# Kernel tuning notes

Hardware: AMD Instinct MI355X
Metric: run time of the kernel (lower is better)

Reference implementation:

```python
import jax, jax.numpy as jnp
import numpy as np

H, W, C_IN, C_OUT, N = 512, 512, 256, 256, 65536


def setup_inputs() -> dict:
    key = jax.random.key(0)
    k1, k2, k3, k4 = jax.random.split(key, 4)
    feature = jax.random.normal(k1, (1, C_IN, H, W), dtype=jnp.float32)
    weight = jax.random.normal(k2, (C_OUT, C_IN, 3, 3), dtype=jnp.float32) * 0.05
    # base sparse locations in the unpadded map; build 3x3 neighborhood indices
    # into the PADDED ([H+2, W+2]) map, exactly like F.pad + fancy indexing.
    base_h = jax.random.randint(k3, (N,), 0, H, dtype=jnp.int32)
    base_w = jax.random.randint(k4, (N,), 0, W, dtype=jnp.int32)
    dh = jnp.repeat(jnp.arange(3, dtype=jnp.int32), 3)  # [9]: 0,0,0,1,1,1,2,2,2
    dw = jnp.tile(jnp.arange(3, dtype=jnp.int32), 3)    # [9]: 0,1,2,0,1,2,...
    h_idx = base_h[None, :] + dh[:, None]  # [9, N], values in [0, H+1]
    w_idx = base_w[None, :] + dw[:, None]  # [9, N], values in [0, W+1]
    return {"feature": feature, "weight": weight, "h_idx": h_idx, "w_idx": w_idx}


def reference(feature, weight, h_idx, w_idx):
    # feature: [1, C, H, W]; weight: [Cout, C, 3, 3]; h_idx/w_idx: [9, N]
    C = feature.shape[1]
    out_ch = weight.shape[0]
    # F.pad(feature, [1,1,1,1])[0] -> [C, H+2, W+2]
    padded = jnp.pad(feature, ((0, 0), (0, 0), (1, 1), (1, 1)))[0]
    # gather 3x3 neighborhoods at sparse locations -> [C, 9, N]
    gathered = padded[:, h_idx, w_idx]
    # .view(9*C, -1): contiguous reshape gives row index c*9 + k
    g = gathered.reshape(C * 9, -1)  # [C*9, N]
    # kernel_d2s = weight.view(out, -1): row ordering c*9 + (kh*3+kw) matches
    k2d = weight.reshape(out_ch, -1)  # [Cout, C*9]
    return k2d @ g  # [Cout, N]
```

## Files before the change

### kernel.cpp

```cpp
#include <hip/hip_runtime.h>
#include <hip/hip_bf16.h>

#define HH 512
#define WW 512
#define CIN 256
#define COUT 256
#define NPTS 65536
#define KTOT 2304
#define PW 514
#define NPIX (PW * PW)

typedef __bf16 bf16x8 __attribute__((ext_vector_type(8)));
typedef float f32x4 __attribute__((ext_vector_type(4)));
typedef unsigned short us8 __attribute__((ext_vector_type(8)));

static __device__ __forceinline__ unsigned short f2bf(float f) {
  unsigned u = __builtin_bit_cast(unsigned, f);
  unsigned r = u + 0x7fffu + ((u >> 16) & 1u);
  return (unsigned short)(r >> 16);
}

static __device__ __forceinline__ void gload16(const void* g, void* l) {
  __builtin_amdgcn_global_load_lds(
      (const __attribute__((address_space(1))) unsigned int*)g,
      (__attribute__((address_space(3))) unsigned int*)l, 16, 0, 0);
}

__global__ __launch_bounds__(256) void prep_weight(const float* __restrict__ w,
                                                   unsigned short* __restrict__ A) {
  int i = blockIdx.x * 256 + threadIdx.x;
  int j  = i & 7;
  int pc = (i >> 3) & 3;
  int co = (i >> 5) & 255;
  int kk = i >> 13;
  int lc = pc ^ ((co >> 1) & 3);
  int k  = kk * 32 + lc * 8 + j;
  int t  = k >> 8;
  int ci = k & 255;
  A[i] = f2bf(w[co * 2304 + ci * 9 + t]);
}

__global__ __launch_bounds__(256) void border_zero(unsigned short* __restrict__ Ft) {
  int g = blockIdx.x * 256 + threadIdx.x;
  if (g >= 2052 * 32) return;
  int p = g >> 5, c = g & 31;
  int py, px;
  if (p < 514)        { py = 0;        px = p; }
  else if (p < 1028)  { py = 513;      px = p - 514; }
  else if (p < 1540)  { py = p - 1027; px = 0; }
  else                { py = p - 1539; px = 513; }
  *(us8*)&Ft[((size_t)py * PW + px) * 256 + c * 8] = (us8){0, 0, 0, 0, 0, 0, 0, 0};
}

__global__ __launch_bounds__(256) void transpose_feat(const float* __restrict__ f,
                                                      unsigned short* __restrict__ Ft) {
  __shared__ unsigned short lds[64 * 264];
  int pix0 = blockIdx.x * 64;
  int y = pix0 >> 9, x0 = pix0 & 511;
  int tid = threadIdx.x;
  int p = tid & 63;
  int cb = tid >> 6;
  const float* src = f + pix0 + p;
  for (int c8 = 0; c8 < 8; ++c8) {
    us8 v;
#pragma unroll
    for (int j = 0; j < 8; ++j) {
      int ci = cb * 64 + c8 * 8 + j;
      v[j] = f2bf(src[ci * 262144]);
    }
    *(us8*)&lds[p * 264 + cb * 64 + c8 * 8] = v;
  }
  __syncthreads();
  int cic = tid & 31;
  int pr = tid >> 5;
  for (int g = 0; g < 8; ++g) {
    int p2 = pr + g * 8;
    us8 v = *(const us8*)&lds[p2 * 264 + cic * 8];
    *(us8*)&Ft[((size_t)((y + 1) * PW + x0 + 1 + p2)) * 256 + cic * 8] = v;
  }
}

__global__ __launch_bounds__(512) void gemm_gather(
    const unsigned short* __restrict__ A,
    const unsigned short* __restrict__ Ft,
    const int* __restrict__ hidx,
    const int* __restrict__ widx,
    float* __restrict__ out) {
  __shared__ unsigned short Asm[2 * 256 * 32];
  __shared__ unsigned short Bsm[2 * 128 * 32];

  int tid = threadIdx.x;
  int n0 = blockIdx.x * 128;
  int lane = tid & 63, wv = tid >> 6;
  int m0 = (wv & 3) * 64;
  int nw0 = (wv >> 2) * 64;

  int col = tid >> 2;
  int pc  = tid & 3;
  int lc  = pc ^ ((col >> 1) & 3);
  int p0  = hidx[n0 + col] * PW + widx[n0 + col];
  const unsigned short* FtT = Ft + (size_t)p0 * 256 + lc * 8;

  f32x4 acc[4][4];
#pragma unroll
  for (int mi = 0; mi < 4; ++mi)
#pragma unroll
    for (int nj = 0; nj < 4; ++nj)
      acc[mi][nj] = (f32x4){0.f, 0.f, 0.f, 0.f};

  unsigned short* AsmW = &Asm[wv * 512];
  unsigned short* BsmW = &Bsm[wv * 512];

#define STAGE(BUF, KK)                                                        \
  do {                                                                        \
    const unsigned short* ga = A + (size_t)(KK) * 8192 + tid * 8;             \
    gload16(ga, AsmW + (BUF) * 8192);                                         \
    gload16(ga + 4096, AsmW + (BUF) * 8192 + 4096);                           \
    int t_ = (KK) >> 3;                                                       \
    int q_ = t_ / 3;                                                          \
    int dt_ = q_ * PW + (t_ - q_ * 3);                                        \
    int ci0_ = ((KK) & 7) * 32;                                               \
    gload16(FtT + (size_t)dt_ * 256 + ci0_, BsmW + (BUF) * 4096);             \
  } while (0)

  STAGE(0, 0);
  __syncthreads();

  int cur = 0;
  for (int kk = 0; kk < 72; ++kk) {
    if (kk + 1 < 72) STAGE(cur ^ 1, kk + 1);

    bf16x8 af[4], bfr[4];
#pragma unroll
    for (int mi = 0; mi < 4; ++mi) {
      int row = m0 + mi * 16 + (lane & 15);
      int ch = (lane >> 4) ^ ((row >> 1) & 3);
      af[mi] = *(const bf16x8*)&Asm[cur * 8192 + row * 32 + ch * 8];
    }
#pragma unroll
    for (int nj = 0; nj < 4; ++nj) {
      int ccol = nw0 + nj * 16 + (lane & 15);
      int ch = (lane >> 4) ^ ((ccol >> 1) & 3);
      bfr[nj] = *(const bf16x8*)&Bsm[cur * 4096 + ccol * 32 + ch * 8];
    }
#pragma unroll
    for (int mi = 0; mi < 4; ++mi)
#pragma unroll
      for (int nj = 0; nj < 4; ++nj)
        acc[mi][nj] = __builtin_amdgcn_mfma_f32_16x16x32_bf16(af[mi], bfr[nj], acc[mi][nj], 0, 0, 0);

    __syncthreads();
    cur ^= 1;
  }
#undef STAGE

  int ocol = n0 + nw0 + (lane & 15);
  int r0 = (lane >> 4) * 4;
#pragma unroll
  for (int mi = 0; mi < 4; ++mi)
#pragma unroll
    for (int nj = 0; nj < 4; ++nj)
#pragma unroll
      for (int r = 0; r < 4; ++r)
        out[(size_t)(m0 + mi * 16 + r0 + r) * NPTS + ocol + nj * 16] = acc[mi][nj][r];
}

__global__ __launch_bounds__(256) void naive_conv(const float* __restrict__ f,
                                                  const float* __restrict__ w,
                                                  const int* __restrict__ hi,
                                                  const int* __restrict__ wi,
                                                  float* __restrict__ out) {
  int idx = blockIdx.x * 256 + threadIdx.x;
  int n = idx & (NPTS - 1);
  int co = idx >> 16;
  int bh = hi[n] - 1;
  int bw = wi[n] - 1;
  float acc = 0.f;
  for (int ci = 0; ci < CIN; ++ci) {
    const float* fc = f + (size_t)ci * 262144;
    const float* wc = w + (size_t)co * 2304 + ci * 9;
#pragma unroll
    for (int t = 0; t < 9; ++t) {
      int y = bh + t / 3, x = bw + t % 3;
      float v = (y >= 0 && y < 512 && x >= 0 && x < 512) ? fc[y * 512 + x] : 0.f;
      acc += wc[t] * v;
    }
  }
  out[(size_t)co * NPTS + n] = acc;
}

extern "C" void kernel_launch(void* const* d_in, const int* in_sizes, int n_in,
                              void* d_out, int out_size, void* d_ws, size_t ws_size,
                              hipStream_t stream) {
  const float* feature = (const float*)d_in[0];
  const float* weight  = (const float*)d_in[1];
  const int* hidx      = (const int*)d_in[2];
  const int* widx      = (const int*)d_in[3];
  float* out           = (float*)d_out;

  const size_t FT_OFF = 2ull * 1024 * 1024;
  const size_t FT_BYTES = (size_t)NPIX * 256 * 2;
  const size_t NEED = FT_OFF + FT_BYTES;

  if (ws_size >= NEED) {
    unsigned short* Abf = (unsigned short*)d_ws;
    unsigned short* Ft = (unsigned short*)((char*)d_ws + FT_OFF);
    prep_weight<<<(72 * 256 * 32) / 256, 256, 0, stream>>>(weight, Abf);
    border_zero<<<(2052 * 32 + 255) / 256, 256, 0, stream>>>(Ft);
    transpose_feat<<<262144 / 64, 256, 0, stream>>>(feature, Ft);
    gemm_gather<<<NPTS / 128, 512, 0, stream>>>(Abf, Ft, hidx, widx, out);
  } else {
    naive_conv<<<(COUT * NPTS) / 256, 256, 0, stream>>>(feature, weight, hidx, widx, out);
  }
}
```

Measured before the change: 191.3 us.

## Enlarge gather-GEMM tile to 256x256 with K=64 steps and interleaved async staging

```diff
diff --git a/kernel.cpp b/kernel.cpp
--- a/kernel.cpp
+++ b/kernel.cpp
@@ -6,9 +6,9 @@
 #define CIN 256
 #define COUT 256
 #define NPTS 65536
-#define KTOT 2304
 #define PW 514
 #define NPIX (PW * PW)
+#define NKT 36
 
 typedef __bf16 bf16x8 __attribute__((ext_vector_type(8)));
 typedef float f32x4 __attribute__((ext_vector_type(4)));
@@ -29,15 +29,17 @@
 __global__ __launch_bounds__(256) void prep_weight(const float* __restrict__ w,
                                                    unsigned short* __restrict__ A) {
   int i = blockIdx.x * 256 + threadIdx.x;
-  int j  = i & 7;
-  int pc = (i >> 3) & 3;
-  int co = (i >> 5) & 255;
-  int kk = i >> 13;
-  int lc = pc ^ ((co >> 1) & 3);
-  int k  = kk * 32 + lc * 8 + j;
+  int kb = i >> 14;
+  int s  = (i >> 13) & 1;
+  int o  = i & 8191;
+  int r  = o >> 5;
+  int cp = (o >> 3) & 3;
+  int j  = o & 7;
+  int c  = cp ^ ((r >> 1) & 3);
+  int k  = kb * 64 + s * 32 + c * 8 + j;
   int t  = k >> 8;
   int ci = k & 255;
-  A[i] = f2bf(w[co * 2304 + ci * 9 + t]);
+  A[i] = f2bf(w[r * 2304 + ci * 9 + t]);
 }
 
 __global__ __launch_bounds__(256) void border_zero(unsigned short* __restrict__ Ft) {
@@ -80,89 +82,152 @@
   }
 }
 
-__global__ __launch_bounds__(512) void gemm_gather(
+__global__ __launch_bounds__(512, 2) void gemm_gather(
     const unsigned short* __restrict__ A,
     const unsigned short* __restrict__ Ft,
     const int* __restrict__ hidx,
     const int* __restrict__ widx,
     float* __restrict__ out) {
-  __shared__ unsigned short Asm[2 * 256 * 32];
-  __shared__ unsigned short Bsm[2 * 128 * 32];
+  __shared__ unsigned short lds[65536];
+  unsigned short* ldsB = lds + 32768;
 
   int tid = threadIdx.x;
-  int n0 = blockIdx.x * 128;
   int lane = tid & 63, wv = tid >> 6;
-  int m0 = (wv & 3) * 64;
-  int nw0 = (wv >> 2) * 64;
-
-  int col = tid >> 2;
-  int pc  = tid & 3;
-  int lc  = pc ^ ((col >> 1) & 3);
-  int p0  = hidx[n0 + col] * PW + widx[n0 + col];
-  const unsigned short* FtT = Ft + (size_t)p0 * 256 + lc * 8;
-
-  f32x4 acc[4][4];
-#pragma unroll
-  for (int mi = 0; mi < 4; ++mi)
+  int wm = wv & 1, wn = wv >> 1;
+  int n0 = blockIdx.x << 8;
+
+  int c0 = tid >> 2;
+  int cc = (tid & 3) ^ ((tid >> 3) & 3);
+  long pixA = (long)hidx[n0 + c0] * PW + widx[n0 + c0];
+  long pixB = (long)hidx[n0 + 128 + c0] * PW + widx[n0 + 128 + c0];
+  const unsigned short* FtB0 = Ft + pixA * 256 + cc * 8;
+  const unsigned short* FtB1 = Ft + pixB * 256 + cc * 8;
+
+#define STAGE_A(dbuf, kb_, s_)                                                \
+  do {                                                                        \
+    const unsigned short* g_ = A + (kb_) * 16384 + (s_) * 8192 + tid * 8;     \
+    unsigned short* l_ = lds + (dbuf) * 16384 + (s_) * 8192 + tid * 8;        \
+    gload16(g_, l_);                                                          \
+    gload16(g_ + 4096, l_ + 4096);                                            \
+  } while (0)
+
+#define STAGE_B(dbuf, s_, base_)                                              \
+  do {                                                                        \
+    unsigned short* l_ = ldsB + (dbuf) * 16384 + (s_) * 8192 + tid * 8;       \
+    gload16(FtB0 + (base_) + (s_) * 32, l_);                                  \
+    gload16(FtB1 + (base_) + (s_) * 32, l_ + 4096);                           \
+  } while (0)
+
+#define LDA(dst, dbuf, s_, mi_)                                               \
+  do {                                                                        \
+    int r_ = wm * 128 + (mi_) * 16 + (lane & 15);                             \
+    int cp_ = (lane >> 4) ^ ((r_ >> 1) & 3);                                  \
+    dst = *(const bf16x8*)&lds[(dbuf) * 16384 + (s_) * 8192 + r_ * 32 + cp_ * 8]; \
+  } while (0)
+
+#define LDB(dst, dbuf, s_, nj_)                                               \
+  do {                                                                        \
+    int col_ = wn * 64 + (nj_) * 16 + (lane & 15);                            \
+    int cp_ = (lane >> 4) ^ ((col_ >> 1) & 3);                                \
+    dst = *(const bf16x8*)&ldsB[(dbuf) * 16384 + (s_) * 8192 + col_ * 32 + cp_ * 8]; \
+  } while (0)
+
+#define MFMA16(mq_)                                                           \
+  do {                                                                        \
+    __builtin_amdgcn_s_setprio(1);                                            \
+    _Pragma("unroll") for (int mi = 0; mi < 4; ++mi)                          \
+        _Pragma("unroll") for (int nj = 0; nj < 4; ++nj)                      \
+            acc[(mq_) * 4 + mi][nj] = __builtin_amdgcn_mfma_f32_16x16x32_bf16( \
+                af[mi], bfr[nj], acc[(mq_) * 4 + mi][nj], 0, 0, 0);           \
+    __builtin_amdgcn_s_setprio(0);                                            \
+  } while (0)
+
+  f32x4 acc[8][4];
+#pragma unroll
+  for (int mi = 0; mi < 8; ++mi)
 #pragma unroll
     for (int nj = 0; nj < 4; ++nj)
       acc[mi][nj] = (f32x4){0.f, 0.f, 0.f, 0.f};
 
-  unsigned short* AsmW = &Asm[wv * 512];
-  unsigned short* BsmW = &Bsm[wv * 512];
-
-#define STAGE(BUF, KK)                                                        \
-  do {                                                                        \
-    const unsigned short* ga = A + (size_t)(KK) * 8192 + tid * 8;             \
-    gload16(ga, AsmW + (BUF) * 8192);                                         \
-    gload16(ga + 4096, AsmW + (BUF) * 8192 + 4096);                           \
-    int t_ = (KK) >> 3;                                                       \
-    int q_ = t_ / 3;                                                          \
-    int dt_ = q_ * PW + (t_ - q_ * 3);                                        \
-    int ci0_ = ((KK) & 7) * 32;                                               \
-    gload16(FtT + (size_t)dt_ * 256 + ci0_, BsmW + (BUF) * 4096);             \
-  } while (0)
-
-  STAGE(0, 0);
-  __syncthreads();
-
-  int cur = 0;
-  for (int kk = 0; kk < 72; ++kk) {
-    if (kk + 1 < 72) STAGE(cur ^ 1, kk + 1);
+  STAGE_A(0, 0, 0);
+  STAGE_B(0, 0, 0);
+  STAGE_A(0, 0, 1);
+  STAGE_B(0, 1, 0);
+  asm volatile("s_waitcnt vmcnt(4)" ::: "memory");
+  __builtin_amdgcn_s_barrier();
+
+  for (int kb = 0; kb < NKT - 1; ++kb) {
+    int d = kb & 1;
+    int kn = kb + 1;
+    int tp = kn >> 2;
+    int q3 = tp / 3;
+    int dtb = (q3 * PW + (tp - q3 * 3)) * 256 + (kn & 3) * 64;
 
     bf16x8 af[4], bfr[4];
-#pragma unroll
-    for (int mi = 0; mi < 4; ++mi) {
-      int row = m0 + mi * 16 + (lane & 15);
-      int ch = (lane >> 4) ^ ((row >> 1) & 3);
-      af[mi] = *(const bf16x8*)&Asm[cur * 8192 + row * 32 + ch * 8];
-    }
-#pragma unroll
-    for (int nj = 0; nj < 4; ++nj) {
-      int ccol = nw0 + nj * 16 + (lane & 15);
-      int ch = (lane >> 4) ^ ((ccol >> 1) & 3);
-      bfr[nj] = *(const bf16x8*)&Bsm[cur * 4096 + ccol * 32 + ch * 8];
-    }
-#pragma unroll
-    for (int mi = 0; mi < 4; ++mi)
-#pragma unroll
-      for (int nj = 0; nj < 4; ++nj)
-        acc[mi][nj] = __builtin_amdgcn_mfma_f32_16x16x32_bf16(af[mi], bfr[nj], acc[mi][nj], 0, 0, 0);
-
-    __syncthreads();
-    cur ^= 1;
-  }
-#undef STAGE
-
-  int ocol = n0 + nw0 + (lane & 15);
+    LDA(af[0], d, 0, 0); LDA(af[1], d, 0, 1); LDA(af[2], d, 0, 2); LDA(af[3], d, 0, 3);
+    LDB(bfr[0], d, 0, 0); LDB(bfr[1], d, 0, 1); LDB(bfr[2], d, 0, 2); LDB(bfr[3], d, 0, 3);
+    STAGE_A(d ^ 1, kn, 0);
+    __builtin_amdgcn_s_barrier();
+    MFMA16(0);
+    __builtin_amdgcn_s_barrier();
+    LDA(af[0], d, 0, 4); LDA(af[1], d, 0, 5); LDA(af[2], d, 0, 6); LDA(af[3], d, 0, 7);
+    STAGE_B(d ^ 1, 0, dtb);
+    __builtin_amdgcn_s_barrier();
+    MFMA16(1);
+    asm volatile("s_waitcnt vmcnt(4)" ::: "memory");
+    __builtin_amdgcn_s_barrier();
+    LDA(af[0], d, 1, 0); LDA(af[1], d, 1, 1); LDA(af[2], d, 1, 2); LDA(af[3], d, 1, 3);
+    LDB(bfr[0], d, 1, 0); LDB(bfr[1], d, 1, 1); LDB(bfr[2], d, 1, 2); LDB(bfr[3], d, 1, 3);
+    STAGE_A(d ^ 1, kn, 1);
+    __builtin_amdgcn_s_barrier();
+    MFMA16(0);
+    __builtin_amdgcn_s_barrier();
+    LDA(af[0], d, 1, 4); LDA(af[1], d, 1, 5); LDA(af[2], d, 1, 6); LDA(af[3], d, 1, 7);
+    STAGE_B(d ^ 1, 1, dtb);
+    __builtin_amdgcn_s_barrier();
+    MFMA16(1);
+    asm volatile("s_waitcnt vmcnt(4)" ::: "memory");
+    __builtin_amdgcn_s_barrier();
+  }
+
+  {
+    const int d = (NKT - 1) & 1;
+    bf16x8 af[4], bfr[4];
+    LDA(af[0], d, 0, 0); LDA(af[1], d, 0, 1); LDA(af[2], d, 0, 2); LDA(af[3], d, 0, 3);
+    LDB(bfr[0], d, 0, 0); LDB(bfr[1], d, 0, 1); LDB(bfr[2], d, 0, 2); LDB(bfr[3], d, 0, 3);
+    __builtin_amdgcn_s_barrier();
+    MFMA16(0);
+    __builtin_amdgcn_s_barrier();
+    LDA(af[0], d, 0, 4); LDA(af[1], d, 0, 5); LDA(af[2], d, 0, 6); LDA(af[3], d, 0, 7);
+    __builtin_amdgcn_s_barrier();
+    MFMA16(1);
+    asm volatile("s_waitcnt vmcnt(0)" ::: "memory");
+    __builtin_amdgcn_s_barrier();
+    LDA(af[0], d, 1, 0); LDA(af[1], d, 1, 1); LDA(af[2], d, 1, 2); LDA(af[3], d, 1, 3);
+    LDB(bfr[0], d, 1, 0); LDB(bfr[1], d, 1, 1); LDB(bfr[2], d, 1, 2); LDB(bfr[3], d, 1, 3);
+    __builtin_amdgcn_s_barrier();
+    MFMA16(0);
+    __builtin_amdgcn_s_barrier();
+    LDA(af[0], d, 1, 4); LDA(af[1], d, 1, 5); LDA(af[2], d, 1, 6); LDA(af[3], d, 1, 7);
+    __builtin_amdgcn_s_barrier();
+    MFMA16(1);
+  }
+
+  int ocol = n0 + wn * 64 + (lane & 15);
   int r0 = (lane >> 4) * 4;
 #pragma unroll
-  for (int mi = 0; mi < 4; ++mi)
+  for (int mi = 0; mi < 8; ++mi)
 #pragma unroll
     for (int nj = 0; nj < 4; ++nj)
 #pragma unroll
       for (int r = 0; r < 4; ++r)
-        out[(size_t)(m0 + mi * 16 + r0 + r) * NPTS + ocol + nj * 16] = acc[mi][nj][r];
+        out[(size_t)(wm * 128 + mi * 16 + r0 + r) * NPTS + ocol + nj * 16] = acc[mi][nj][r];
+
+#undef STAGE_A
+#undef STAGE_B
+#undef LDA
+#undef LDB
+#undef MFMA16
 }
 
 __global__ __launch_bounds__(256) void naive_conv(const float* __restrict__ f,
@@ -205,10 +270,10 @@
   if (ws_size >= NEED) {
     unsigned short* Abf = (unsigned short*)d_ws;
     unsigned short* Ft = (unsigned short*)((char*)d_ws + FT_OFF);
-    prep_weight<<<(72 * 256 * 32) / 256, 256, 0, stream>>>(weight, Abf);
+    prep_weight<<<(NKT * 16384) / 256, 256, 0, stream>>>(weight, Abf);
     border_zero<<<(2052 * 32 + 255) / 256, 256, 0, stream>>>(Ft);
     transpose_feat<<<262144 / 64, 256, 0, stream>>>(feature, Ft);
-    gemm_gather<<<NPTS / 128, 512, 0, stream>>>(Abf, Ft, hidx, widx, out);
+    gemm_gather<<<NPTS / 256, 512, 0, stream>>>(Abf, Ft, hidx, widx, out);
   } else {
     naive_conv<<<(COUT * NPTS) / 256, 256, 0, stream>>>(feature, weight, hidx, widx, out);
   }
```

Measured after the change: 176.0 us. 1.09x faster.
